# Kernel optimization log

Measured on AMD Instinct MI355X. Metric: run time of the kernel, lower is better.

The kernel has to match this reference:

```python
import jax, jax.numpy as jnp
import numpy as np

# sparse_shape = grid_size[::-1] + [1,0,0] for grid_size=[1408,1600,40]
Z, Y, X = 41, 1600, 1408
N = 400000
CIN, COUT = 4, 16
EPS = 1e-3  # BatchNorm1d eps from partial(nn.BatchNorm1d, eps=0.001)


def setup_inputs() -> dict:
    # unique active voxel coordinates (submanifold conv assumes no duplicates)
    rng = np.random.default_rng(0)
    pool = Z * Y * X
    raw = rng.integers(0, pool, size=3 * N, dtype=np.int64)
    lin = np.unique(raw)[:N]
    assert lin.size == N
    z = lin // (Y * X)
    rem = lin % (Y * X)
    y = rem // X
    x = rem % X
    coords = np.stack([np.zeros(N, np.int64), z, y, x], axis=1).astype(np.int32)

    key = jax.random.key(0)
    k1, k2 = jax.random.split(key)
    voxel_features = jax.random.normal(k1, (N, CIN), dtype=jnp.float32)
    # SubMConv3d weight: one [CIN,COUT] matrix per kernel offset (27 = 3^3)
    weight = jax.random.normal(k2, (27, CIN, COUT), dtype=jnp.float32) * 0.1
    gamma = jnp.ones((COUT,), dtype=jnp.float32)
    beta = jnp.zeros((COUT,), dtype=jnp.float32)
    return {
        "voxel_features": voxel_features,
        "voxel_coords": jnp.asarray(coords),
        "weight": weight,
        "gamma": gamma,
        "beta": beta,
    }


_OFFSETS = jnp.asarray(
    np.stack(np.meshgrid([-1, 0, 1], [-1, 0, 1], [-1, 0, 1], indexing="ij"), -1
             ).reshape(27, 3),
    dtype=jnp.int32,
)


def _subm_conv(feats, coords, weight):
    """Submanifold sparse 3D conv: outputs only at active voxel sites.

    Rulebook built via sorted linear keys + searchsorted (gather-GEMM).
    """
    zyx = coords[:, 1:4].astype(jnp.int32)                 # [N,3]
    keys = (zyx[:, 0] * Y + zyx[:, 1]) * X + zyx[:, 2]     # [N] unique linear key
    order = jnp.argsort(keys)
    skeys = keys[order]

    nb = zyx[None, :, :] + _OFFSETS[:, None, :]            # [27,N,3]
    inb = ((nb >= 0).all(-1)
           & (nb[..., 0] < Z) & (nb[..., 1] < Y) & (nb[..., 2] < X))
    nkeys = (nb[..., 0] * Y + nb[..., 1]) * X + nb[..., 2]  # [27,N]
    pos = jnp.clip(jnp.searchsorted(skeys, nkeys), 0, N - 1)
    found = inb & (skeys[pos] == nkeys)                    # neighbor is active
    idx = order[pos]                                       # [27,N] row into feats

    gathered = jnp.where(found[..., None], feats[idx], 0.0)  # [27,N,CIN]
    return jnp.einsum("knc,kco->no", gathered, weight)       # [N,COUT]


def reference(voxel_features, voxel_coords, weight, gamma, beta):
    out = _subm_conv(voxel_features, voxel_coords, weight)
    # BatchNorm1d in training mode: normalize over the N (voxel) axis
    mu = out.mean(0)
    var = out.var(0)
    out = (out - mu) * jax.lax.rsqrt(var + EPS) * gamma + beta
    return jax.nn.relu(out)
```

## Files before the change

kernel.cpp:

```cpp
#include <hip/hip_runtime.h>
#include <stdint.h>

#define ZD 41
#define YD 1600
#define XD 1408
#define YXD (YD * XD)
#define NKEYS (ZD * YD * XD)
#define BM_WORDS ((NKEYS + 63) / 64)
#define BN_EPS 1e-3f

typedef unsigned long long u64;


__global__ void __launch_bounds__(256) build_index(
    const int4* __restrict__ coords, uint32_t* __restrict__ prefix,
    u64* __restrict__ bitmap, int n) {
  int i = blockIdx.x * blockDim.x + threadIdx.x;

  {
    int4 cl = coords[n - 1];
    int wlast = ((cl.y * YD + cl.z) * XD + cl.w) >> 6;
    int stride = gridDim.x * blockDim.x;
    for (int g = wlast + 1 + i; g < BM_WORDS; g += stride) {
      bitmap[g] = 0ull;
      prefix[g] = (uint32_t)n;
    }
  }

  if (i >= n) return;
  int4 c = coords[i];
  int key = (c.y * YD + c.z) * XD + c.w;
  int w = key >> 6;
  int pw = -1;
  if (i > 0) {
    int4 cp = coords[i - 1];
    pw = ((cp.y * YD + cp.z) * XD + cp.w) >> 6;
  }
  if (w != pw) {
    for (int g = pw + 1; g < w; ++g) {
      bitmap[g] = 0ull;
      prefix[g] = (uint32_t)i;
    }
    u64 bits = 1ull << (key & 63);
    int j = i + 1;
    while (j < n) {
      int4 cj = coords[j];
      int kj = (cj.y * YD + cj.z) * XD + cj.w;
      if ((kj >> 6) != w) break;
      bits |= 1ull << (kj & 63);
      ++j;
    }
    bitmap[w] = bits;
    prefix[w] = (uint32_t)i;
  }
}

__global__ void __launch_bounds__(256) subm_conv(
    const float4* __restrict__ feats, const int4* __restrict__ coords,
    const float* __restrict__ weight, const uint32_t* __restrict__ prefix,
    const u64* __restrict__ bitmap, float* __restrict__ out,
    float* __restrict__ partial, int n) {
  __shared__ float wl[27 * 64];
  __shared__ float sw[4][32];
  for (int t = threadIdx.x; t < 27 * 64; t += 256) wl[t] = weight[t];
  __syncthreads();

  int B = gridDim.x;
  int q = B >> 3, r = B & 7;
  int xcd = blockIdx.x & 7, off = blockIdx.x >> 3;
  int sb = (xcd < r ? xcd * (q + 1) : r * (q + 1) + (xcd - r) * q) + off;
  int i = sb * 256 + (int)threadIdx.x;

  float acc[16];
#pragma unroll
  for (int o = 0; o < 16; o++) acc[o] = 0.f;

  if (i < n) {
    int4 czyx = coords[i];
    int z = czyx.y, y = czyx.z, x = czyx.w;
    int key = (z * YD + y) * XD + x;

#pragma unroll
    for (int dz = -1; dz <= 1; dz++) {
      if ((unsigned)(z + dz) >= (unsigned)ZD) continue;
#pragma unroll
      for (int dy = -1; dy <= 1; dy++) {
        if ((unsigned)(y + dy) >= (unsigned)YD) continue;
        int nb = key + dz * YXD + dy * XD;
        int base = nb - 1;
        int w0i = base >> 6;
        u64 w0 = bitmap[w0i];
        u64 w1 = bitmap[w0i + 1];
        unsigned p = (unsigned)(base & 63);
        u64 win = (w0 >> p) | (p ? (w1 << (64 - p)) : 0ull);
        unsigned m = (unsigned)win & 7u;
        if (x == 0) m &= 6u;
        if (x == XD - 1) m &= 3u;
        if (!m) continue;
        uint32_t pre0 = prefix[w0i];
        uint32_t pre1 = prefix[w0i + 1];
        do {
          int b = __ffs(m) - 1;
          m &= m - 1;
          int nk = base + b;
          int wi = nk >> 6;
          u64 word = (wi == w0i) ? w0 : w1;
          uint32_t pre = (wi == w0i) ? pre0 : pre1;
          int j = (int)pre + __popcll(word & ((1ull << (nk & 63)) - 1ull));
          float4 f = feats[j];
          const float* wp = &wl[((dz + 1) * 9 + (dy + 1) * 3 + b) * 64];
#pragma unroll
          for (int o = 0; o < 16; o++)
            acc[o] += f.x * wp[o] + f.y * wp[o + 16] + f.z * wp[o + 32] +
                      f.w * wp[o + 48];
        } while (m);
      }
    }

    float4* o4 = (float4*)(out + (size_t)i * 16);
    o4[0] = make_float4(acc[0], acc[1], acc[2], acc[3]);
    o4[1] = make_float4(acc[4], acc[5], acc[6], acc[7]);
    o4[2] = make_float4(acc[8], acc[9], acc[10], acc[11]);
    o4[3] = make_float4(acc[12], acc[13], acc[14], acc[15]);
  }

  int lane = threadIdx.x & 63, wv = threadIdx.x >> 6;
#pragma unroll
  for (int o = 0; o < 16; o++) {
    float s = acc[o], qq = acc[o] * acc[o];
#pragma unroll
    for (int offx = 32; offx; offx >>= 1) {
      s += __shfl_xor(s, offx);
      qq += __shfl_xor(qq, offx);
    }
    if (lane == 0) {
      sw[wv][o] = s;
      sw[wv][16 + o] = qq;
    }
  }
  __syncthreads();
  if (threadIdx.x < 32) {
    float v = sw[0][threadIdx.x] + sw[1][threadIdx.x] + sw[2][threadIdx.x] +
              sw[3][threadIdx.x];
    partial[(size_t)blockIdx.x * 32 + threadIdx.x] = v;
  }
}

__global__ void __launch_bounds__(1024) bn_finalize(
    const float4* __restrict__ partial4, float* __restrict__ accum, int nb) {
  __shared__ float4 s4[1024];
  int t = threadIdx.x;
  int q = t & 7;
  int row0 = t >> 3;
  float4 v = make_float4(0.f, 0.f, 0.f, 0.f);
  for (int b = row0; b < nb; b += 128) {
    float4 p = partial4[(size_t)b * 8 + q];
    v.x += p.x;
    v.y += p.y;
    v.z += p.z;
    v.w += p.w;
  }
  s4[t] = v;
  __syncthreads();
  for (int half = 64; half >= 1; half >>= 1) {
    if (row0 < half) {
      float4 o = s4[t + half * 8];
      v.x += o.x;
      v.y += o.y;
      v.z += o.z;
      v.w += o.w;
      s4[t] = v;
    }
    __syncthreads();
  }
  if (t < 8) ((float4*)accum)[t] = s4[t];
}

__global__ void __launch_bounds__(256) bn_apply(
    float* __restrict__ out, const float* __restrict__ accum,
    const float* __restrict__ gamma, const float* __restrict__ beta, int n4,
    float invN) {
  __shared__ float sa[16], sb[16];
  int t = threadIdx.x;
  if (t < 16) {
    float mu = accum[t] * invN;
    float var = accum[16 + t] * invN - mu * mu;
    float inv = rsqrtf(var + BN_EPS);
    float a = gamma[t] * inv;
    sa[t] = a;
    sb[t] = beta[t] - mu * a;
  }
  __syncthreads();
  int i = blockIdx.x * 256 + t;
  if (i >= n4) return;
  float4* p = (float4*)out;
  float4 v = p[i];
  int c0 = (i & 3) * 4;
  v.x = fmaxf(v.x * sa[c0 + 0] + sb[c0 + 0], 0.f);
  v.y = fmaxf(v.y * sa[c0 + 1] + sb[c0 + 1], 0.f);
  v.z = fmaxf(v.z * sa[c0 + 2] + sb[c0 + 2], 0.f);
  v.w = fmaxf(v.w * sa[c0 + 3] + sb[c0 + 3], 0.f);
  p[i] = v;
}

extern "C" void kernel_launch(void* const* d_in, const int* in_sizes, int n_in,
                              void* d_out, int out_size, void* d_ws,
                              size_t ws_size, hipStream_t stream) {
  const float4* feats = (const float4*)d_in[0];
  const int4* coords = (const int4*)d_in[1];
  const float* weight = (const float*)d_in[2];
  const float* gamma = (const float*)d_in[3];
  const float* beta = (const float*)d_in[4];
  int n = in_sizes[0] / 4;

  float* accum = (float*)d_ws;
  uint32_t* prefix = (uint32_t*)((char*)d_ws + 128);
  u64* bitmap = (u64*)((char*)d_ws + 128 + (size_t)BM_WORDS * 4);
  float* partial =
      (float*)((char*)d_ws + 128 + (size_t)BM_WORDS * 4 + (size_t)BM_WORDS * 8 + 8);

  int bb = (n + 255) / 256;
  hipLaunchKernelGGL(build_index, dim3(bb), dim3(256), 0, stream, coords,
                     prefix, bitmap, n);
  hipLaunchKernelGGL(subm_conv, dim3(bb), dim3(256), 0, stream, feats, coords,
                     weight, prefix, bitmap, (float*)d_out, partial, n);
  hipLaunchKernelGGL(bn_finalize, dim3(1), dim3(1024), 0, stream,
                     (const float4*)partial, accum, bb);
  int n4 = n * 4;
  hipLaunchKernelGGL(bn_apply, dim3((n4 + 255) / 256), dim3(256), 0, stream,
                     (float*)d_out, accum, gamma, beta, n4, 1.0f / n);
}
```

Baseline: 129.5 us.

## Pack 32-bit occupancy bits with prefix counts into single 64-bit entries

Replaces the separate 64-bit bitmap and 32-bit prefix arrays with one array of 64-bit entries, each holding a 32-bit occupancy mask and its prefix count, so a neighbour lookup needs one load instead of two. The conv kernel first builds a 27-bit neighbour mask from all nine z/y rows, then loops over the set bits with flat indexing, and handles the centre voxel directly without a lookup. The build kernel reads the previous key through a wave shuffle instead of a global load. The index is twice as many words and the conv loop now re-reads an entry per found neighbour, trading some extra memory traffic for fewer dependent loads and less branch divergence.

```diff
diff --git a/kernel.cpp b/kernel.cpp
--- a/kernel.cpp
+++ b/kernel.cpp
@@ -6,62 +6,57 @@
 #define XD 1408
 #define YXD (YD * XD)
 #define NKEYS (ZD * YD * XD)
-#define BM_WORDS ((NKEYS + 63) / 64)
+#define ENT_WORDS (NKEYS / 32)
 #define BN_EPS 1e-3f
 
 typedef unsigned long long u64;
 
 
 __global__ void __launch_bounds__(256) build_index(
-    const int4* __restrict__ coords, uint32_t* __restrict__ prefix,
-    u64* __restrict__ bitmap, int n) {
+    const int4* __restrict__ coords, u64* __restrict__ entry, int n) {
   int i = blockIdx.x * blockDim.x + threadIdx.x;
 
   {
     int4 cl = coords[n - 1];
-    int wlast = ((cl.y * YD + cl.z) * XD + cl.w) >> 6;
+    int glast = (((cl.y * YD + cl.z) * XD + cl.w)) >> 5;
     int stride = gridDim.x * blockDim.x;
-    for (int g = wlast + 1 + i; g < BM_WORDS; g += stride) {
-      bitmap[g] = 0ull;
-      prefix[g] = (uint32_t)n;
-    }
+    for (int g = glast + 1 + i; g < ENT_WORDS; g += stride)
+      entry[g] = (u64)(uint32_t)n;
   }
 
   if (i >= n) return;
   int4 c = coords[i];
   int key = (c.y * YD + c.z) * XD + c.w;
-  int w = key >> 6;
-  int pw = -1;
-  if (i > 0) {
+  int g = key >> 5;
+
+  int pkey = __shfl_up(key, 1);
+  if ((threadIdx.x & 63) == 0 && i > 0) {
     int4 cp = coords[i - 1];
-    pw = ((cp.y * YD + cp.z) * XD + cp.w) >> 6;
-  }
-  if (w != pw) {
-    for (int g = pw + 1; g < w; ++g) {
-      bitmap[g] = 0ull;
-      prefix[g] = (uint32_t)i;
-    }
-    u64 bits = 1ull << (key & 63);
+    pkey = (cp.y * YD + cp.z) * XD + cp.w;
+  }
+  int pg = (i > 0) ? (pkey >> 5) : -1;
+
+  if (g != pg) {
+    for (int gg = pg + 1; gg < g; ++gg) entry[gg] = (u64)(uint32_t)i;
+    uint32_t bits = 1u << (key & 31);
     int j = i + 1;
     while (j < n) {
       int4 cj = coords[j];
       int kj = (cj.y * YD + cj.z) * XD + cj.w;
-      if ((kj >> 6) != w) break;
-      bits |= 1ull << (kj & 63);
+      if ((kj >> 5) != g) break;
+      bits |= 1u << (kj & 31);
       ++j;
     }
-    bitmap[w] = bits;
-    prefix[w] = (uint32_t)i;
+    entry[g] = ((u64)bits << 32) | (uint32_t)i;
   }
 }
 
 __global__ void __launch_bounds__(256) subm_conv(
     const float4* __restrict__ feats, const int4* __restrict__ coords,
-    const float* __restrict__ weight, const uint32_t* __restrict__ prefix,
-    const u64* __restrict__ bitmap, float* __restrict__ out,
-    float* __restrict__ partial, int n) {
+    const float* __restrict__ weight, const u64* __restrict__ entry,
+    float* __restrict__ out, float* __restrict__ partial, int n) {
   __shared__ float wl[27 * 64];
-  __shared__ float sw[4][32];
+  __shared__ float swred[4][32];
   for (int t = threadIdx.x; t < 27 * 64; t += 256) wl[t] = weight[t];
   __syncthreads();
 
@@ -80,41 +75,54 @@
     int z = czyx.y, y = czyx.z, x = czyx.w;
     int key = (z * YD + y) * XD + x;
 
-#pragma unroll
-    for (int dz = -1; dz <= 1; dz++) {
-      if ((unsigned)(z + dz) >= (unsigned)ZD) continue;
-#pragma unroll
-      for (int dy = -1; dy <= 1; dy++) {
-        if ((unsigned)(y + dy) >= (unsigned)YD) continue;
-        int nb = key + dz * YXD + dy * XD;
-        int base = nb - 1;
-        int w0i = base >> 6;
-        u64 w0 = bitmap[w0i];
-        u64 w1 = bitmap[w0i + 1];
-        unsigned p = (unsigned)(base & 63);
-        u64 win = (w0 >> p) | (p ? (w1 << (64 - p)) : 0ull);
-        unsigned m = (unsigned)win & 7u;
-        if (x == 0) m &= 6u;
-        if (x == XD - 1) m &= 3u;
-        if (!m) continue;
-        uint32_t pre0 = prefix[w0i];
-        uint32_t pre1 = prefix[w0i + 1];
-        do {
-          int b = __ffs(m) - 1;
-          m &= m - 1;
-          int nk = base + b;
-          int wi = nk >> 6;
-          u64 word = (wi == w0i) ? w0 : w1;
-          uint32_t pre = (wi == w0i) ? pre0 : pre1;
-          int j = (int)pre + __popcll(word & ((1ull << (nk & 63)) - 1ull));
-          float4 f = feats[j];
-          const float* wp = &wl[((dz + 1) * 9 + (dy + 1) * 3 + b) * 64];
-#pragma unroll
-          for (int o = 0; o < 16; o++)
-            acc[o] += f.x * wp[o] + f.y * wp[o + 16] + f.z * wp[o + 32] +
-                      f.w * wp[o + 48];
-        } while (m);
+    {
+      float4 fs = feats[i];
+      const float* wp = &wl[13 * 64];
+#pragma unroll
+      for (int o = 0; o < 16; o++)
+        acc[o] = fs.x * wp[o] + fs.y * wp[o + 16] + fs.z * wp[o + 32] +
+                 fs.w * wp[o + 48];
+    }
+
+    unsigned mask27 = 0;
+#pragma unroll
+    for (int dzy = 0; dzy < 9; dzy++) {
+      const int dz = dzy / 3 - 1, dy = dzy % 3 - 1;
+      bool ok = ((unsigned)(z + dz) < (unsigned)ZD) &&
+                ((unsigned)(y + dy) < (unsigned)YD);
+      int base = key + dz * YXD + dy * XD - 1;
+      int g0 = base >> 5;
+      u64 e0 = 0, e1 = 0;
+      if (ok) {
+        e0 = entry[g0];
+        e1 = entry[g0 + 1];
       }
+      u64 W = (e0 >> 32) | (e1 & 0xFFFFFFFF00000000ull);
+      unsigned m3 = (unsigned)(W >> (base & 31)) & 7u;
+      mask27 |= m3 << (dzy * 3);
+    }
+    mask27 &= ~(1u << 13);
+    if (x == 0) mask27 &= ~0x1249249u;
+    if (x == XD - 1) mask27 &= ~0x4924924u;
+
+    while (mask27) {
+      int b = __ffs(mask27) - 1;
+      mask27 &= mask27 - 1;
+      int dzy = (b * 11) >> 5;
+      int rem = b - dzy * 3;
+      int dzq = (dzy * 11) >> 5;
+      int dyr = dzy - dzq * 3;
+      int s = key + (dzq - 1) * YXD + (dyr - 1) * XD + rem - 1;
+      int gs = s >> 5;
+      u64 e = entry[gs];
+      int j = (int)(e & 0xFFFFFFFFull) +
+              __popc((uint32_t)(e >> 32) & ((1u << (s & 31)) - 1u));
+      float4 f = feats[j];
+      const float* wp = &wl[b * 64];
+#pragma unroll
+      for (int o = 0; o < 16; o++)
+        acc[o] += f.x * wp[o] + f.y * wp[o + 16] + f.z * wp[o + 32] +
+                  f.w * wp[o + 48];
     }
 
     float4* o4 = (float4*)(out + (size_t)i * 16);
@@ -134,14 +142,14 @@
       qq += __shfl_xor(qq, offx);
     }
     if (lane == 0) {
-      sw[wv][o] = s;
-      sw[wv][16 + o] = qq;
+      swred[wv][o] = s;
+      swred[wv][16 + o] = qq;
     }
   }
   __syncthreads();
   if (threadIdx.x < 32) {
-    float v = sw[0][threadIdx.x] + sw[1][threadIdx.x] + sw[2][threadIdx.x] +
-              sw[3][threadIdx.x];
+    float v = swred[0][threadIdx.x] + swred[1][threadIdx.x] +
+              swred[2][threadIdx.x] + swred[3][threadIdx.x];
     partial[(size_t)blockIdx.x * 32 + threadIdx.x] = v;
   }
 }
@@ -214,16 +222,14 @@
   int n = in_sizes[0] / 4;
 
   float* accum = (float*)d_ws;
-  uint32_t* prefix = (uint32_t*)((char*)d_ws + 128);
-  u64* bitmap = (u64*)((char*)d_ws + 128 + (size_t)BM_WORDS * 4);
-  float* partial =
-      (float*)((char*)d_ws + 128 + (size_t)BM_WORDS * 4 + (size_t)BM_WORDS * 8 + 8);
+  u64* entry = (u64*)((char*)d_ws + 256);
+  float* partial = (float*)((char*)d_ws + 256 + (size_t)ENT_WORDS * 8 + 16);
 
   int bb = (n + 255) / 256;
   hipLaunchKernelGGL(build_index, dim3(bb), dim3(256), 0, stream, coords,
-                     prefix, bitmap, n);
+                     entry, n);
   hipLaunchKernelGGL(subm_conv, dim3(bb), dim3(256), 0, stream, feats, coords,
-                     weight, prefix, bitmap, (float*)d_out, partial, n);
+                     weight, entry, (float*)d_out, partial, n);
   hipLaunchKernelGGL(bn_finalize, dim3(1), dim3(1024), 0, stream,
                      (const float4*)partial, accum, bb);
   int n4 = n * 4;
```

New measurement: 123.8 us. 4.3% less time.
